# Kernel optimization log

Hardware: AMD Instinct MI355X
Metric: run time of the kernel (lower is better)

Reference implementation:

```python
import jax, jax.numpy as jnp
import numpy as np

DIM = 2048
ORDER = 1
# upper-triangular index pairs (i<j), row-major over i then j — matches torch loop order
_IU_ROWS, _IU_COLS = np.triu_indices(DIM, k=1)


def setup_inputs() -> dict:
    key = jax.random.key(0)
    k1, k2 = jax.random.split(key)
    num_params = DIM * (DIM - 1) // 2
    x = jax.random.normal(k1, (4, 4096, DIM), dtype=jnp.float32)
    angles = jax.random.normal(k2, (num_params,), dtype=jnp.float32) * 0.01
    bias = jnp.zeros((DIM,), dtype=jnp.float32)
    return {"x": x, "angles": angles, "bias": bias}


def _skew_symmetric(angles):
    # A[i,j] = angles[k], A[j,i] = -angles[k] for upper-tri (i<j)
    A = jnp.zeros((DIM, DIM), dtype=angles.dtype)
    A = A.at[_IU_ROWS, _IU_COLS].set(angles)
    return A - A.T


def _cayley_approx(A, order=ORDER):
    # W = (I + A + ... + A^order) @ (I + A)
    I = jnp.eye(DIM, dtype=A.dtype)
    inv_approx = I
    A_power = A
    for _ in range(order):
        inv_approx = inv_approx + A_power
        A_power = A_power @ A
    return inv_approx @ (I + A)


def reference(x, angles, bias):
    A = _skew_symmetric(angles)
    W = _cayley_approx(A)
    # [b, s, d] @ [d, d] -> [b, s, d]
    out = jnp.einsum('bsd,de->bse', x, W) + bias
    return out
```

## Files before the change

### kernel.cpp

```cpp
#include <hip/hip_runtime.h>
#include <stdint.h>

#define DIM 2048

typedef short short8 __attribute__((ext_vector_type(8)));
typedef float f32x4 __attribute__((ext_vector_type(4)));

__device__ __forceinline__ unsigned short f2bf(float f) {
    union { float f; unsigned int u; } v;
    v.f = f;
    unsigned int r = v.u + 0x7FFFu + ((v.u >> 16) & 1u);
    return (unsigned short)(r >> 16);
}
__device__ __forceinline__ float bf2f(unsigned short u) {
    union { unsigned int u; float f; } v;
    v.u = ((unsigned int)u) << 16;
    return v.f;
}

__device__ __forceinline__ void async16(const unsigned short* g, unsigned short* l) {
    __builtin_amdgcn_global_load_lds(
        (__attribute__((address_space(1))) void*)(uintptr_t)g,
        (__attribute__((address_space(3))) void*)(uintptr_t)l,
        16, 0, 0);
}

__global__ __launch_bounds__(256) void build_A_tiled(const float* __restrict__ ang,
                                                     unsigned short* __restrict__ A) {
    __shared__ float tile[64][65];
    int b = blockIdx.x;
    int ti = 0, rem = b;
    while (rem >= 32 - ti) { rem -= 32 - ti; ++ti; }
    const int tj = ti + rem;
    const int t  = threadIdx.x;
    const int lj = t & 63;
    const int lw = t >> 6;
    const bool diag = (ti == tj);

#pragma unroll
    for (int m = 0; m < 16; ++m) {
        const int li = lw * 16 + m;
        const int i = ti * 64 + li;
        const int j = tj * 64 + lj;
        float v = 0.0f;
        if (i < j) v = ang[i * (4095 - i) / 2 + (j - i - 1)];
        tile[li][lj] = v;
    }
    __syncthreads();

#pragma unroll
    for (int m = 0; m < 16; ++m) {
        const int li = lw * 16 + m;
        float v;
        if (diag) {
            if (li < lj)      v =  tile[li][lj];
            else if (li > lj) v = -tile[lj][li];
            else              v = 0.0f;
        } else {
            v = tile[li][lj];
        }
        A[(size_t)(ti * 64 + li) * DIM + tj * 64 + lj] = f2bf(v);
    }
    if (!diag) {
#pragma unroll
        for (int m = 0; m < 16; ++m) {
            const int li = lw * 16 + m;
            A[(size_t)(tj * 64 + li) * DIM + ti * 64 + lj] = f2bf(-tile[lj][li]);
        }
    }
}

__global__ void cvt_f32_bf16(const float* __restrict__ in, unsigned short* __restrict__ out) {
    int i = (blockIdx.x * 256 + threadIdx.x) * 4;
    const float4 v = *(const float4*)(in + i);
    ushort4 o;
    o.x = f2bf(v.x); o.y = f2bf(v.y); o.z = f2bf(v.z); o.w = f2bf(v.w);
    *(ushort4*)(out + i) = o;
}

__global__ __launch_bounds__(256) void gemm_s64(
        const unsigned short* __restrict__ A,
        unsigned short* __restrict__ Wt) {
    __shared__ __align__(16) unsigned short ldsA[64 * 64];
    __shared__ __align__(16) unsigned short ldsB[64 * 64];
    const int K = DIM, N = DIM;

    const int t    = threadIdx.x;
    const int flat = blockIdx.y * 32 + blockIdx.x;
    const int swz  = (flat & 7) * 128 + (flat >> 3);
    const int bn   = (swz & 31) * 64;
    const int bm   = (swz >> 5) * 64;
    const int lane = t & 63;
    const int wave = t >> 6;
    const int waveM = (wave >> 1) * 32;
    const int waveN = (wave & 1) * 32;
    const int fm = lane & 15;
    const int fq = lane >> 4;

    f32x4 acc[2][2];
#pragma unroll
    for (int i = 0; i < 2; ++i)
#pragma unroll
        for (int j = 0; j < 2; ++j)
            acc[i][j] = (f32x4){0.f, 0.f, 0.f, 0.f};

    const int trow   = t >> 3;
    const int tchunk = (t & 7) ^ (trow & 7);
    const unsigned short* gA = A + (size_t)(bm + trow) * K + tchunk * 8;
    const unsigned short* gB = A + (size_t)(bn + trow) * K + tchunk * 8;
    const size_t rowskip = (size_t)32 * K;
    unsigned short* lA = ldsA + t * 8;
    unsigned short* lB = ldsB + t * 8;

    for (int kt = 0; kt < K; kt += 64) {
        __syncthreads();
        async16(gA + kt, lA);
        async16(gA + kt + rowskip, lA + 2048);
        async16(gB + kt, lB);
        async16(gB + kt + rowskip, lB + 2048);
        __syncthreads();

#pragma unroll
        for (int ks = 0; ks < 2; ++ks) {
            short8 af[2], bfv[2];
#pragma unroll
            for (int i = 0; i < 2; ++i) {
                const int rowA = waveM + i * 16 + fm;
                const int rowB = waveN + i * 16 + fm;
                af[i]  = *(const short8*)(ldsA + rowA * 64 + (((ks << 2) + fq) ^ (rowA & 7)) * 8);
                bfv[i] = *(const short8*)(ldsB + rowB * 64 + (((ks << 2) + fq) ^ (rowB & 7)) * 8);
            }
#pragma unroll
            for (int i = 0; i < 2; ++i)
#pragma unroll
                for (int j = 0; j < 2; ++j)
                    acc[i][j] = __builtin_amdgcn_mfma_f32_16x16x32_bf16(
                        af[i], bfv[j], acc[i][j], 0, 0, 0);
        }
    }

#pragma unroll
    for (int i = 0; i < 2; ++i) {
#pragma unroll
        for (int j = 0; j < 2; ++j) {
            const int col = bn + waveN + j * 16 + fm;
#pragma unroll
            for (int r = 0; r < 4; ++r) {
                const int row = bm + waveM + i * 16 + fq * 4 + r;
                const float a = bf2f(A[(size_t)row * N + col]);
                const float w = (row == col ? 1.0f : 0.0f) - 2.0f * a - acc[i][j][r];
                Wt[(size_t)row * N + col] = f2bf(w);
            }
        }
    }
}


#define WAITV(N) asm volatile("s_waitcnt vmcnt(" #N ")" ::: "memory")
#define BAR() do { asm volatile("" ::: "memory"); __builtin_amdgcn_s_barrier(); asm volatile("" ::: "memory"); } while (0)

#define STG_A(BUF, R0, KT) async16(gA + (size_t)(R0) * 2048 + (KT), &ldsA[BUF][(R0) * 64 + t * 8])
#define STG_B(BUF, R0, KT) async16(gB + (size_t)(R0) * 2048 + (KT), &ldsB[BUF][(R0) * 64 + t * 8])

#define READ_A_(BUF, IH) do { \
    _Pragma("unroll") \
    for (int ii = 0; ii < 4; ++ii) { \
        const int row  = waveM + (IH) * 64 + ii * 16 + fm; \
        const int base = row * 64; \
        af[ii][0] = *(const short8*)(&ldsA[BUF][base + ((fq    ) ^ (row & 7)) * 8]); \
        af[ii][1] = *(const short8*)(&ldsA[BUF][base + ((fq + 4) ^ (row & 7)) * 8]); \
    } } while (0)

#define READ_B_(BUF, JH) do { \
    _Pragma("unroll") \
    for (int jj = 0; jj < 2; ++jj) { \
        const int row  = (JH) * 128 + wn * 32 + jj * 16 + fm; \
        const int base = row * 64; \
        bfr[JH][jj][0] = *(const short8*)(&ldsB[BUF][base + ((fq    ) ^ (row & 7)) * 8]); \
        bfr[JH][jj][1] = *(const short8*)(&ldsB[BUF][base + ((fq + 4) ^ (row & 7)) * 8]); \
    } } while (0)

#define MMAQ(IH, JH) do { \
    __builtin_amdgcn_s_setprio(1); \
    _Pragma("unroll") \
    for (int ks = 0; ks < 2; ++ks) \
    _Pragma("unroll") \
    for (int ii = 0; ii < 4; ++ii) \
    _Pragma("unroll") \
    for (int jj = 0; jj < 2; ++jj) \
        acc[(IH) * 4 + ii][(JH) * 2 + jj] = __builtin_amdgcn_mfma_f32_16x16x32_bf16( \
            af[ii][ks], bfr[JH][jj][ks], acc[(IH) * 4 + ii][(JH) * 2 + jj], 0, 0, 0); \
    __builtin_amdgcn_s_setprio(0); \
} while (0)

#define TILE(BUF, KTN, PRE, VN, NXT) do { \
     \
    BAR(); \
    if (PRE) { STG_A(BUF, 0, KTN); STG_A(BUF, 128, KTN); STG_B(BUF, 0, KTN); STG_B(BUF, 64, KTN); } \
    MMAQ(0, 0); \
    READ_B_(BUF, 1); \
     \
    BAR(); \
    if (PRE) { STG_B(BUF, 128, KTN); STG_B(BUF, 192, KTN); } \
    MMAQ(0, 1); \
    READ_A_(BUF, 1); \
     \
    WAITV(VN); \
    BAR(); \
    if (PRE) { STG_A(BUF, 64, KTN); STG_A(BUF, 192, KTN); } \
    MMAQ(1, 0); \
    if (NXT) READ_B_((BUF) ^ 1, 0); \
     \
    BAR(); \
    MMAQ(1, 1); \
    if (NXT) READ_A_((BUF) ^ 1, 0); \
} while (0)

#define TILE_LAST(BUF) do { \
    BAR(); MMAQ(0, 0); READ_B_(BUF, 1); \
    BAR(); MMAQ(0, 1); READ_A_(BUF, 1); \
    BAR(); MMAQ(1, 0); \
    MMAQ(1, 1); \
} while (0)

__global__ __launch_bounds__(512, 2) void gemm_main(
        const unsigned short* __restrict__ Aop,
        const unsigned short* __restrict__ Bop,
        int M, int N, int K,
        const float* __restrict__ bias,
        float* __restrict__ out) {
    __shared__ __align__(16) unsigned short ldsA[2][256 * 64];
    __shared__ __align__(16) unsigned short ldsB[2][256 * 64];

    const int t    = threadIdx.x;
    const int flat = blockIdx.y * 8 + blockIdx.x;
    const int swz  = (flat & 7) * 64 + (flat >> 3);
    const int bn   = (swz & 7) * 256;
    const int bm   = (swz >> 3) * 256;
    const int lane = t & 63;
    const int wave = t >> 6;
    const int wm   = wave >> 2;
    const int wn   = wave & 3;
    const int waveM = wm * 128;
    const int fm = lane & 15;
    const int fq = lane >> 4;

    f32x4 acc[8][4];
#pragma unroll
    for (int i = 0; i < 8; ++i)
#pragma unroll
        for (int j = 0; j < 4; ++j)
            acc[i][j] = (f32x4){0.f, 0.f, 0.f, 0.f};

    short8 af[4][2];
    short8 bfr[2][2][2];

    const int trow   = t >> 3;
    const int tchunk = (t & 7) ^ (trow & 7);
    const unsigned short* gA = Aop + (size_t)(bm + trow) * 2048 + tchunk * 8;
    const unsigned short* gB = Bop + (size_t)(bn + trow) * 2048 + tchunk * 8;

    STG_A(0, 0, 0);   STG_A(0, 128, 0);  STG_B(0, 0, 0);   STG_B(0, 64, 0);
    STG_B(0, 128, 0); STG_B(0, 192, 0);  STG_A(0, 64, 0);  STG_A(0, 192, 0);
    STG_A(1, 0, 64);  STG_A(1, 128, 64); STG_B(1, 0, 64);  STG_B(1, 64, 64);
    STG_B(1, 128, 64);STG_B(1, 192, 64); STG_A(1, 64, 64); STG_A(1, 192, 64);
    WAITV(8);
    BAR();
    READ_A_(0, 0);
    READ_B_(0, 0);

#pragma unroll 1
    for (int it = 0; it < 15; ++it) {
        const int kt = it * 128;
        TILE(0, kt + 128, 1, 6, 1);
        TILE(1, kt + 192, 1, 6, 1);
    }
    TILE(0, 0, 0, 0, 1);
    TILE_LAST(1);

#pragma unroll
    for (int i = 0; i < 8; ++i) {
        const int row0 = bm + waveM + i * 16 + fq * 4;
#pragma unroll
        for (int j = 0; j < 4; ++j) {
            const int col = bn + (j >> 1) * 128 + wn * 32 + (j & 1) * 16 + fm;
            const float b = bias[col];
#pragma unroll
            for (int r = 0; r < 4; ++r)
                out[(size_t)(row0 + r) * 2048 + col] = acc[i][j][r] + b;
        }
    }
}

extern "C" void kernel_launch(void* const* d_in, const int* in_sizes, int n_in,
                              void* d_out, int out_size, void* d_ws, size_t ws_size,
                              hipStream_t stream) {
    const float* x      = (const float*)d_in[0];
    const float* angles = (const float*)d_in[1];
    const float* bias   = (const float*)d_in[2];
    float* out = (float*)d_out;

    char* ws = (char*)d_ws;
    unsigned short* Abf = (unsigned short*)ws;
    unsigned short* Wt  = (unsigned short*)(ws + (8u << 20));
    unsigned short* xbf = (unsigned short*)(ws + (16u << 20));

    const int M = 4 * 4096;
    const int n_elem_x = M * DIM;

    build_A_tiled<<<528, 256, 0, stream>>>(angles, Abf);
    cvt_f32_bf16<<<(n_elem_x / 4) / 256, 256, 0, stream>>>(x, xbf);

    gemm_s64<<<dim3(DIM / 64, DIM / 64), 256, 0, stream>>>(Abf, Wt);

    gemm_main<<<dim3(DIM / 256, M / 256), 512, 0, stream>>>(
        xbf, Wt, M, DIM, DIM, bias, out);
}
```

Baseline: 371.3 us.

## Exploit symmetry of A^2 to compute half the tiles and fuse x conversion

Since A is skew-symmetric, A·A is symmetric. The A² GEMM now computes only the 528 upper-triangular 64x64 tiles and writes each mirrored tile of W through an LDS transpose, using W = I - 2A - A² and its transpose I + 2A - A². The separate x fp32-to-bf16 conversion kernel is folded into the same launch as extra blocks, which removes one launch. The cost is a triangular index search per block, an extra LDS transpose pass, and mixing two unrelated workloads in one grid.

```diff
diff --git a/kernel.cpp b/kernel.cpp
--- a/kernel.cpp
+++ b/kernel.cpp
@@ -70,26 +70,34 @@
     }
 }
 
-__global__ void cvt_f32_bf16(const float* __restrict__ in, unsigned short* __restrict__ out) {
-    int i = (blockIdx.x * 256 + threadIdx.x) * 4;
-    const float4 v = *(const float4*)(in + i);
-    ushort4 o;
-    o.x = f2bf(v.x); o.y = f2bf(v.y); o.z = f2bf(v.z); o.w = f2bf(v.w);
-    *(ushort4*)(out + i) = o;
-}
-
-__global__ __launch_bounds__(256) void gemm_s64(
+__global__ __launch_bounds__(256) void s64sym_cvt(
         const unsigned short* __restrict__ A,
-        unsigned short* __restrict__ Wt) {
-    __shared__ __align__(16) unsigned short ldsA[64 * 64];
-    __shared__ __align__(16) unsigned short ldsB[64 * 64];
+        unsigned short* __restrict__ Wt,
+        const float* __restrict__ x,
+        unsigned short* __restrict__ xbf) {
+    __shared__ __align__(16) unsigned short smem[12288];
+    unsigned short* ldsA = smem;
+    unsigned short* ldsB = smem + 4096;
+    float* ldsT = (float*)smem;
+
+    if (blockIdx.x >= 528) {
+        const int i = ((blockIdx.x - 528) * 256 + threadIdx.x) * 4;
+        const float4 v = *(const float4*)(x + i);
+        ushort4 o;
+        o.x = f2bf(v.x); o.y = f2bf(v.y); o.z = f2bf(v.z); o.w = f2bf(v.w);
+        *(ushort4*)(xbf + i) = o;
+        return;
+    }
+
     const int K = DIM, N = DIM;
-
-    const int t    = threadIdx.x;
-    const int flat = blockIdx.y * 32 + blockIdx.x;
-    const int swz  = (flat & 7) * 128 + (flat >> 3);
-    const int bn   = (swz & 31) * 64;
-    const int bm   = (swz >> 5) * 64;
+    const int t = threadIdx.x;
+    const int swz = (blockIdx.x & 7) * 66 + (blockIdx.x >> 3);
+    int ti = 0, rem = swz;
+    while (rem >= 32 - ti) { rem -= 32 - ti; ++ti; }
+    const int tj = ti + rem;
+    const int bm = ti * 64;
+    const int bn = tj * 64;
+
     const int lane = t & 63;
     const int wave = t >> 6;
     const int waveM = (wave >> 1) * 32;
@@ -139,19 +147,35 @@
         }
     }
 
+    __syncthreads();
 #pragma unroll
     for (int i = 0; i < 2; ++i) {
 #pragma unroll
         for (int j = 0; j < 2; ++j) {
-            const int col = bn + waveN + j * 16 + fm;
+            const int lj = waveN + j * 16 + fm;
+            const int gj = bn + lj;
 #pragma unroll
             for (int r = 0; r < 4; ++r) {
-                const int row = bm + waveM + i * 16 + fq * 4 + r;
-                const float a = bf2f(A[(size_t)row * N + col]);
-                const float w = (row == col ? 1.0f : 0.0f) - 2.0f * a - acc[i][j][r];
-                Wt[(size_t)row * N + col] = f2bf(w);
+                const int li = waveM + i * 16 + fq * 4 + r;
+                const int gi = bm + li;
+                const float a = bf2f(A[(size_t)gi * N + gj]);
+                const float s = acc[i][j][r];
+                const float d = (gi == gj) ? 1.0f : 0.0f;
+                Wt[(size_t)gi * N + gj] = f2bf(d - 2.0f * a - s);
+                ldsT[lj * 65 + li] = d + 2.0f * a - s;
             }
         }
+    }
+    __syncthreads();
+    {
+        const int r  = t >> 2;
+        const int cb = (t & 3) * 16;
+        unsigned short o[16];
+#pragma unroll
+        for (int u = 0; u < 16; ++u)
+            o[u] = f2bf(ldsT[r * 65 + cb + u]);
+        *(short8*)(Wt + (size_t)(bn + r) * N + bm + cb)     = *(short8*)(o);
+        *(short8*)(Wt + (size_t)(bn + r) * N + bm + cb + 8) = *(short8*)(o + 8);
     }
 }
 
@@ -306,12 +330,10 @@
     unsigned short* xbf = (unsigned short*)(ws + (16u << 20));
 
     const int M = 4 * 4096;
-    const int n_elem_x = M * DIM;
 
     build_A_tiled<<<528, 256, 0, stream>>>(angles, Abf);
-    cvt_f32_bf16<<<(n_elem_x / 4) / 256, 256, 0, stream>>>(x, xbf);
-
-    gemm_s64<<<dim3(DIM / 64, DIM / 64), 256, 0, stream>>>(Abf, Wt);
+
+    s64sym_cvt<<<528 + 32768, 256, 0, stream>>>(Abf, Wt, x, xbf);
 
     gemm_main<<<dim3(DIM / 256, M / 256), 512, 0, stream>>>(
         xbf, Wt, M, DIM, DIM, bias, out);
```

Measured after the change: 349.6 us. 5.9% less time.
